# Kernel tuning notes

Hardware: AMD Instinct MI355X
Metric: run time of the kernel (lower is better)

Reference implementation:

```python
import jax, jax.numpy as jnp
import numpy as np

BLOCK_SIZE = 256
N_EMBD = 768
HEAD_SIZE = 768  # == n_embd so RoPE table (dim=n_embd) matches channel pairing


def _rope_tables(T, dim, theta0=10000.0):
    # compute_freq(dim=n_embd, seq_len=block_size, theta_0=10000):
    # theta_j = theta0^(-2j/dim), angle[t, j] = t * theta_j
    j = jnp.arange(dim // 2, dtype=jnp.float32)
    theta = jnp.float32(theta0) ** (-2.0 * j / jnp.float32(dim))
    ang = jnp.arange(T, dtype=jnp.float32)[:, None] * theta[None, :]  # [T, dim/2]
    return jnp.cos(ang), jnp.sin(ang)


def _apply_rope(t, cos, sin):
    # t: [B, T, D]; pair adjacent channels (2j, 2j+1) as complex, rotate.
    B, T, D = t.shape
    tr = t.reshape(B, T, D // 2, 2)
    re, im = tr[..., 0], tr[..., 1]
    out_re = re * cos[None] - im * sin[None]
    out_im = re * sin[None] + im * cos[None]
    return jnp.stack([out_re, out_im], axis=-1).reshape(B, T, D)


def setup_inputs() -> dict:
    key = jax.random.key(0)
    k1, k2, k3, k4 = jax.random.split(key, 4)
    B, T = 128, BLOCK_SIZE
    x = jax.random.normal(k1, (B, T, N_EMBD), dtype=jnp.float32)
    Wq = jax.random.normal(k2, (N_EMBD, HEAD_SIZE), dtype=jnp.float32) * 0.02
    Wk = jax.random.normal(k3, (N_EMBD, HEAD_SIZE), dtype=jnp.float32) * 0.02
    Wv = jax.random.normal(k4, (N_EMBD, HEAD_SIZE), dtype=jnp.float32) * 0.02
    return {"x": x, "Wq": Wq, "Wk": Wk, "Wv": Wv}


def reference(x, Wq, Wk, Wv):
    B, T, C = x.shape
    q = x @ Wq  # [B, T, D]
    k = x @ Wk
    v = x @ Wv
    cos, sin = _rope_tables(T, HEAD_SIZE)
    q = _apply_rope(q, cos, sin)
    k = _apply_rope(k, cos, sin)
    scale = jnp.float32(HEAD_SIZE) ** -0.5
    wei = jnp.einsum('bqd,bkd->bqk', q, k) * scale  # [B, T, T]
    causal = jnp.tril(jnp.ones((T, T), dtype=bool))
    wei = jnp.where(causal[None], wei, -jnp.inf)
    wei = jax.nn.softmax(wei, axis=-1)
    # dropout(p=0.2) is identity in eval/deterministic baseline
    out = jnp.einsum('bqk,bkd->bqd', wei, v)  # [B, T, D]
    return out
```

## Files before the change

### kernel.cpp

```cpp
#include <hip/hip_runtime.h>
#include <hip/hip_bf16.h>
#include <stdint.h>


typedef __attribute__((ext_vector_type(8))) short short8;
typedef __attribute__((ext_vector_type(4))) short short4v;
typedef __attribute__((ext_vector_type(4))) float f32x4;

__device__ __forceinline__ short f2bf(float f) {
    uint32_t u = __float_as_uint(f);
    u += 0x7fffu + ((u >> 16) & 1u);
    return (short)(u >> 16);
}

__global__ __launch_bounds__(256) void cvt_x(const float* __restrict__ x,
                                             short* __restrict__ xb) {
    long i = ((long)blockIdx.x * 256 + threadIdx.x) * 4;
    f32x4 v = *(const f32x4*)(x + i);
    short4v o;
    o.x = f2bf(v.x); o.y = f2bf(v.y); o.z = f2bf(v.z); o.w = f2bf(v.w);
    *(short4v*)(xb + i) = o;
}

__global__ __launch_bounds__(256) void cvt_wt(const float* __restrict__ W,
                                              short* __restrict__ Wt) {
    __shared__ float tile[32][33];
    int d0 = blockIdx.x * 32, c0 = blockIdx.y * 32;
    int tr = threadIdx.x >> 5, tc = threadIdx.x & 31;
    #pragma unroll
    for (int i = 0; i < 32; i += 8)
        tile[tr + i][tc] = W[(long)(c0 + tr + i) * 768 + d0 + tc];
    __syncthreads();
    #pragma unroll
    for (int i = 0; i < 32; i += 8)
        Wt[(long)(d0 + tr + i) * 768 + c0 + tc] = f2bf(tile[tc][tr + i]);
}

__global__ __launch_bounds__(256) void rope_tab(float2* __restrict__ rt) {
    int i = blockIdx.x * 256 + threadIdx.x;
    int t = i / 384, j = i - t * 384;
    const float CE = -0.034603417655f;
    float th = exp2f((float)j * CE);
    float s, c;
    sincosf((float)t * th, &s, &c);
    rt[i] = make_float2(c, s);
}

__global__ __launch_bounds__(512, 2)
void qkv256(const short* __restrict__ A, const short* __restrict__ B,
            short* __restrict__ Q, short* __restrict__ Kb,
            short* __restrict__ Vt, const float2* __restrict__ rt) {
    int p = blockIdx.x;
    int c = p & 7, j = p >> 3;
    int st = j / 9;
    int bx = j - st * 9;
    int by = c * 16 + st;
    const int m0 = by * 256, n0 = bx * 256;

    __shared__ short lA[2][256 * 64];
    __shared__ short lB[2][256 * 64];

    const int tid = threadIdx.x;
    const int w = tid >> 6, lane = tid & 63;
    const int wm = (w >> 2) * 128;
    const int wn = (w & 3) * 64;
    const int lr8 = lane >> 3;
    const int scol = (((lane & 7) - lr8) & 7) * 8;
    const int fr = lane & 15, kq = lane >> 4;

    f32x4 acc[8][4] = {};
    short8 af[4][2];
    short8 bq[4][2];

#define STAGE_HALF(lX, gX, r0g, h, t) do {                                     \
    int _buf = (t) & 1;                                                        \
    _Pragma("unroll")                                                          \
    for (int _i = 0; _i < 2; ++_i) {                                           \
        int _rl = (h) * 128 + (w * 2 + _i) * 8;                                \
        const short* _g = (gX) + (long)((r0g) + _rl + lr8) * 768               \
                               + (t) * 64 + scol;                              \
        __builtin_amdgcn_global_load_lds(                                      \
            (const __attribute__((address_space(1))) void*)_g,                 \
            (__attribute__((address_space(3))) void*)(&lX[_buf][_rl * 64]),    \
            16, 0, 0);                                                         \
    }                                                                          \
} while (0)

#define LOAD_A(mh, buf) do {                                                   \
    _Pragma("unroll")                                                          \
    for (int _t = 0; _t < 4; ++_t)                                             \
        _Pragma("unroll")                                                      \
        for (int _k = 0; _k < 2; ++_k)                                         \
            af[_t][_k] = *(const short8*)(&lA[buf][                            \
                (wm + (mh) * 64 + _t * 16 + fr) * 64 +                         \
                ((_k * 4 + kq + fr) & 7) * 8]);                                \
} while (0)

#define LOAD_B(nh, buf) do {                                                   \
    _Pragma("unroll")                                                          \
    for (int _t = 0; _t < 2; ++_t)                                             \
        _Pragma("unroll")                                                      \
        for (int _k = 0; _k < 2; ++_k)                                         \
            bq[(nh) * 2 + _t][_k] = *(const short8*)(&lB[buf][                 \
                (wn + (nh) * 32 + _t * 16 + fr) * 64 +                         \
                ((_k * 4 + kq + fr) & 7) * 8]);                                \
} while (0)

#define MMA_Q(mh, nh) do {                                                     \
    __builtin_amdgcn_s_setprio(1);                                             \
    _Pragma("unroll")                                                          \
    for (int _t = 0; _t < 4; ++_t)                                             \
        _Pragma("unroll")                                                      \
        for (int _n = 0; _n < 2; ++_n)                                         \
            _Pragma("unroll")                                                  \
            for (int _k = 0; _k < 2; ++_k)                                     \
                acc[(mh) * 4 + _t][(nh) * 2 + _n] =                            \
                    __builtin_amdgcn_mfma_f32_16x16x32_bf16(                   \
                        af[_t][_k], bq[(nh) * 2 + _n][_k],                     \
                        acc[(mh) * 4 + _t][(nh) * 2 + _n], 0, 0, 0);           \
    __builtin_amdgcn_s_setprio(0);                                             \
} while (0)

#define BAR() __builtin_amdgcn_s_barrier()
#define LGKM0() asm volatile("s_waitcnt lgkmcnt(0)" ::: "memory")
#define VMC4() asm volatile("s_waitcnt vmcnt(4)" ::: "memory")
#define VMC0() asm volatile("s_waitcnt vmcnt(0)" ::: "memory")

    STAGE_HALF(lB, B, n0, 0, 0);
    STAGE_HALF(lB, B, n0, 1, 0);
    STAGE_HALF(lA, A, m0, 0, 0);
    STAGE_HALF(lA, A, m0, 1, 0);
    STAGE_HALF(lB, B, n0, 0, 1);
    STAGE_HALF(lB, B, n0, 1, 1);
    VMC4();
    BAR();

    #pragma unroll 1
    for (int i = 0; i < 6; ++i) {
        const int t0 = 2 * i;
        const bool more = (i < 5);
        LOAD_A(0, 0); LOAD_B(0, 0);
        STAGE_HALF(lA, A, m0, 0, t0 + 1);
        BAR(); LGKM0(); MMA_Q(0, 0); BAR();
        LOAD_B(1, 0);
        STAGE_HALF(lA, A, m0, 1, t0 + 1);
        BAR(); LGKM0(); MMA_Q(0, 1); BAR();
        LOAD_A(1, 0);
        if (more) STAGE_HALF(lB, B, n0, 0, t0 + 2);
        BAR(); LGKM0(); MMA_Q(1, 1); BAR();
        if (more) { STAGE_HALF(lB, B, n0, 1, t0 + 2); VMC4(); }
        else      { VMC0(); }
        BAR(); LGKM0(); MMA_Q(1, 0); BAR();
        LOAD_A(0, 1); LOAD_B(0, 1);
        if (more) STAGE_HALF(lA, A, m0, 0, t0 + 2);
        BAR(); LGKM0(); MMA_Q(0, 0); BAR();
        LOAD_B(1, 1);
        if (more) STAGE_HALF(lA, A, m0, 1, t0 + 2);
        BAR(); LGKM0(); MMA_Q(0, 1); BAR();
        LOAD_A(1, 1);
        if (more) STAGE_HALF(lB, B, n0, 0, t0 + 3);
        BAR(); LGKM0(); MMA_Q(1, 1); BAR();
        if (more) { STAGE_HALF(lB, B, n0, 1, t0 + 3); VMC4(); }
        BAR(); LGKM0(); MMA_Q(1, 0); BAR();
    }

    const int type = (bx >= 6) ? 2 : (bx >= 3 ? 1 : 0);
    const int nl0 = n0 - type * 768;
    const int r0 = wm + (lane >> 4) * 4;
    const int c0 = wn + (lane & 15);
    if (type < 2) {
        short* dst = (type == 0) ? Q : Kb;
        const int par = lane & 1;
        #pragma unroll
        for (int tmi = 0; tmi < 8; ++tmi)
            #pragma unroll
            for (int tni = 0; tni < 4; ++tni) {
                int col = nl0 + c0 + tni * 16;
                const float2* rtc = rt + (col >> 1);
                #pragma unroll
                for (int r = 0; r < 4; ++r) {
                    int row = m0 + r0 + tmi * 16 + r;
                    float val = acc[tmi][tni][r];
                    float pv = __shfl_xor(val, 1);
                    float2 cs = rtc[(row & 255) * 384];
                    float re = par ? pv : val;
                    float im = par ? val : pv;
                    float o = par ? (re * cs.y + im * cs.x)
                                  : (re * cs.x - im * cs.y);
                    dst[(long)row * 768 + col] = f2bf(o);
                }
            }
    } else {
        #pragma unroll
        for (int tmi = 0; tmi < 8; ++tmi)
            #pragma unroll
            for (int tni = 0; tni < 4; ++tni) {
                int col = nl0 + c0 + tni * 16;
                #pragma unroll
                for (int r = 0; r < 4; ++r) {
                    int row = m0 + r0 + tmi * 16 + r;
                    Vt[((long)(row >> 8) * 768 + col) * 256 + (row & 255)] =
                        f2bf(acc[tmi][tni][r]);
                }
            }
    }
#undef STAGE_HALF
#undef LOAD_A
#undef LOAD_B
#undef MMA_Q
#undef BAR
#undef LGKM0
#undef VMC4
#undef VMC0
}

template <int EPI, int CAUSAL, int SWZ>
__global__ __launch_bounds__(256)
void gemm_bt(const short* __restrict__ A, const short* __restrict__ B,
             void* __restrict__ C, void* __restrict__ C2, void* __restrict__ C3,
             const float2* __restrict__ rt,
             int M, int N, int K, long sA, long sB, long sC, float scale) {
    int bx, by, bz;
    if (SWZ == 2) {
        int p = blockIdx.x + 2 * (blockIdx.y + 2 * blockIdx.z);
        int c = p & 7, j = p >> 3;
        bz = c * 16 + (j >> 2);
        by = (j >> 1) & 1; bx = j & 1;
    } else if (SWZ == 3) {
        int p = blockIdx.x + 6 * (blockIdx.y + 2 * blockIdx.z);
        int c = p & 7, j = p >> 3;
        int bt = j / 12;
        bz = c * 16 + bt;
        int t = j - bt * 12;
        by = t / 6; bx = t - (t / 6) * 6;
    } else {
        bx = blockIdx.x; by = blockIdx.y; bz = blockIdx.z;
    }
    const int m0 = by * 128;
    const int n0 = bx * 128;
    if (CAUSAL == 1 && n0 > m0) return;

    __shared__ short lA[128 * 64];
    __shared__ short lB[128 * 64];
    const short* Ab = A + (long)bz * sA;
    const short* Bb = B + (long)bz * sB;
    const int tid = threadIdx.x;
    const int w = tid >> 6, lane = tid & 63;
    const int wm = (w >> 1) * 64;
    const int wn = (w & 1) * 64;
    const int lrow8 = lane >> 3;
    const int lcol = (((lane & 7) - lrow8) & 7) * 8;
    const int fr = lane & 15;
    const int kq = lane >> 4;

    const int Kend = (CAUSAL == 2) ? (m0 + 128 < K ? m0 + 128 : K) : K;

    f32x4 acc[4][4] = {};

    for (int k0 = 0; k0 < Kend; k0 += 64) {
        #pragma unroll
        for (int i = 0; i < 4; ++i) {
            int seg = i * 4 + w;
            int row = seg * 8 + lrow8;
            const short* ga = Ab + (long)(m0 + row) * K + k0 + lcol;
            __builtin_amdgcn_global_load_lds(
                (const __attribute__((address_space(1))) void*)ga,
                (__attribute__((address_space(3))) void*)(lA + seg * 512),
                16, 0, 0);
            const short* gb = Bb + (long)(n0 + row) * K + k0 + lcol;
            __builtin_amdgcn_global_load_lds(
                (const __attribute__((address_space(1))) void*)gb,
                (__attribute__((address_space(3))) void*)(lB + seg * 512),
                16, 0, 0);
        }
        __syncthreads();

        #pragma unroll
        for (int c = 0; c < 2; ++c) {
            const int sphys = ((c * 4 + kq + fr) & 7) * 8;
            short8 afr[4], bfr[4];
            #pragma unroll
            for (int tmi = 0; tmi < 4; ++tmi)
                afr[tmi] = *(const short8*)(lA + (wm + fr + tmi * 16) * 64 + sphys);
            #pragma unroll
            for (int tni = 0; tni < 4; ++tni)
                bfr[tni] = *(const short8*)(lB + (wn + fr + tni * 16) * 64 + sphys);
            #pragma unroll
            for (int tmi = 0; tmi < 4; ++tmi)
                #pragma unroll
                for (int tni = 0; tni < 4; ++tni)
                    acc[tmi][tni] = __builtin_amdgcn_mfma_f32_16x16x32_bf16(
                        afr[tmi], bfr[tni], acc[tmi][tni], 0, 0, 0);
        }
        __syncthreads();
    }

    const int r0 = wm + (lane >> 4) * 4;
    const int c0 = wn + (lane & 15);

    if (EPI == 2) {
        #pragma unroll
        for (int tmi = 0; tmi < 4; ++tmi)
            #pragma unroll
            for (int tni = 0; tni < 4; ++tni)
                #pragma unroll
                for (int r = 0; r < 4; ++r) {
                    int row = m0 + r0 + tmi * 16 + r;
                    int col = n0 + c0 + tni * 16;
                    ((float*)C)[(long)bz * sC + (long)row * N + col] =
                        acc[tmi][tni][r] * scale;
                }
    }
}

__global__ __launch_bounds__(256) void softmax_p(const float* __restrict__ S,
                                                 short* __restrict__ P) {
    int wv = threadIdx.x >> 6, lane = threadIdx.x & 63;
    int row = blockIdx.x * 4 + wv;
    int t = row & 255;
    f32x4 v = *(const f32x4*)(S + (long)row * 256 + lane * 4);
    float vals[4];
    float m = -1e30f;
    #pragma unroll
    for (int j = 0; j < 4; ++j) {
        int n = lane * 4 + j;
        vals[j] = (n <= t) ? v[j] : -1e30f;
        m = fmaxf(m, vals[j]);
    }
    #pragma unroll
    for (int o = 32; o; o >>= 1) m = fmaxf(m, __shfl_xor(m, o));
    float e[4], sum = 0.f;
    #pragma unroll
    for (int j = 0; j < 4; ++j) { e[j] = __expf(vals[j] - m); sum += e[j]; }
    #pragma unroll
    for (int o = 32; o; o >>= 1) sum += __shfl_xor(sum, o);
    float inv = 1.0f / sum;
    short4v o4;
    o4.x = f2bf(e[0] * inv); o4.y = f2bf(e[1] * inv);
    o4.z = f2bf(e[2] * inv); o4.w = f2bf(e[3] * inv);
    *(short4v*)(P + (long)row * 256 + lane * 4) = o4;
}

extern "C" void kernel_launch(void* const* d_in, const int* in_sizes, int n_in,
                              void* d_out, int out_size, void* d_ws, size_t ws_size,
                              hipStream_t stream) {
    const float* x  = (const float*)d_in[0];
    const float* Wq = (const float*)d_in[1];
    const float* Wk = (const float*)d_in[2];
    const float* Wv = (const float*)d_in[3];

    char* ws = (char*)d_ws;
    short*  xb = (short*)(ws);
    short*  wt = (short*)(ws + 50331648);
    short*  qb = (short*)(ws + 53870592);
    short*  kb = (short*)(ws + 104202240);
    short*  vt = (short*)(ws + 154533888);
    float*  S  = (float*)(ws + 204865536);
    short*  P  = (short*)(ws + 238419968);
    float2* rt = (float2*)(ws + 255197184);

    cvt_x<<<24576, 256, 0, stream>>>(x, xb);
    dim3 gw(24, 24);
    cvt_wt<<<gw, 256, 0, stream>>>(Wq, wt);
    cvt_wt<<<gw, 256, 0, stream>>>(Wk, wt + 589824);
    cvt_wt<<<gw, 256, 0, stream>>>(Wv, wt + 1179648);
    rope_tab<<<384, 256, 0, stream>>>(rt);

    qkv256<<<1152, 512, 0, stream>>>(xb, wt, qb, kb, vt, rt);

    dim3 g2(2, 2, 128);
    gemm_bt<2, 1, 2><<<g2, 256, 0, stream>>>(qb, kb, S, nullptr, nullptr, nullptr,
                                             256, 256, 768, 196608, 196608, 65536,
                                             0.0360843918f);

    softmax_p<<<8192, 256, 0, stream>>>(S, P);

    dim3 g3(6, 2, 128);
    gemm_bt<2, 2, 3><<<g3, 256, 0, stream>>>(P, vt, (float*)d_out, nullptr,
                                             nullptr, nullptr, 256, 768, 256,
                                             65536, 196608, 196608, 1.0f);
}
```

Measured before the change: 412.5 us.

## Fuse QK^T score GEMM with causal softmax into one kernel

Replaces the separate causal QK^T GEMM (which wrote fp32 scores) and the row-softmax kernel with one kernel. Each 512-thread block computes a 128x256 score tile, masks it, and does the row max and sum reductions through LDS before writing bf16 probabilities. This removes the fp32 S round trip through global memory and one launch, but the block computes the fully masked upper tile instead of skipping it, and only 256 blocks are launched. The QKV GEMM loop also moves its vmcnt wait to after the last MFMA quarter so loads overlap more compute.

Result: no change. 412.1 us (-0.1%).

```diff
diff --git a/kernel.cpp b/kernel.cpp
--- a/kernel.cpp
+++ b/kernel.cpp
@@ -148,9 +148,10 @@
         LOAD_A(1, 0);
         if (more) STAGE_HALF(lB, B, n0, 0, t0 + 2);
         BAR(); LGKM0(); MMA_Q(1, 1); BAR();
-        if (more) { STAGE_HALF(lB, B, n0, 1, t0 + 2); VMC4(); }
-        else      { VMC0(); }
-        BAR(); LGKM0(); MMA_Q(1, 0); BAR();
+        if (more) STAGE_HALF(lB, B, n0, 1, t0 + 2);
+        BAR(); LGKM0(); MMA_Q(1, 0);
+        if (more) { VMC4(); } else { VMC0(); }
+        BAR();
         LOAD_A(0, 1); LOAD_B(0, 1);
         if (more) STAGE_HALF(lA, A, m0, 0, t0 + 2);
         BAR(); LGKM0(); MMA_Q(0, 0); BAR();
@@ -160,8 +161,10 @@
         LOAD_A(1, 1);
         if (more) STAGE_HALF(lB, B, n0, 0, t0 + 3);
         BAR(); LGKM0(); MMA_Q(1, 1); BAR();
-        if (more) { STAGE_HALF(lB, B, n0, 1, t0 + 3); VMC4(); }
-        BAR(); LGKM0(); MMA_Q(1, 0); BAR();
+        if (more) STAGE_HALF(lB, B, n0, 1, t0 + 3);
+        BAR(); LGKM0(); MMA_Q(1, 0);
+        if (more) VMC4();
+        BAR();
     }
 
     const int type = (bx >= 6) ? 2 : (bx >= 3 ? 1 : 0);
@@ -214,6 +217,153 @@
 #undef VMC0
 }
 
+__global__ __launch_bounds__(512)
+void s_softmax(const short* __restrict__ Qm, const short* __restrict__ Km,
+               short* __restrict__ P, float scale) {
+    int p = blockIdx.x;
+    int c = p & 7, j = p >> 3;
+    int bz = c * 16 + (j >> 1);
+    int mh = j & 1;
+    const short* Ab = Qm + (long)bz * 196608 + (long)mh * 98304;
+    const short* Bb = Km + (long)bz * 196608;
+
+    __shared__ short lA[128 * 64];
+    __shared__ short lB[256 * 64];
+
+    const int tid = threadIdx.x;
+    const int w = tid >> 6, lane = tid & 63;
+    const int wm = (w >> 2) * 64;
+    const int wn = (w & 3) * 64;
+    const int lr8 = lane >> 3;
+    const int scol = (((lane & 7) - lr8) & 7) * 8;
+    const int fr = lane & 15, kq = lane >> 4;
+
+    f32x4 acc[4][4] = {};
+
+    for (int k0 = 0; k0 < 768; k0 += 64) {
+        #pragma unroll
+        for (int i = 0; i < 2; ++i) {
+            int seg = i * 8 + w;
+            const short* ga = Ab + (long)(seg * 8 + lr8) * 768 + k0 + scol;
+            __builtin_amdgcn_global_load_lds(
+                (const __attribute__((address_space(1))) void*)ga,
+                (__attribute__((address_space(3))) void*)(lA + seg * 512),
+                16, 0, 0);
+        }
+        #pragma unroll
+        for (int i = 0; i < 4; ++i) {
+            int seg = i * 8 + w;
+            const short* gb = Bb + (long)(seg * 8 + lr8) * 768 + k0 + scol;
+            __builtin_amdgcn_global_load_lds(
+                (const __attribute__((address_space(1))) void*)gb,
+                (__attribute__((address_space(3))) void*)(lB + seg * 512),
+                16, 0, 0);
+        }
+        __syncthreads();
+        #pragma unroll
+        for (int cc = 0; cc < 2; ++cc) {
+            const int sphys = ((cc * 4 + kq + fr) & 7) * 8;
+            short8 afr[4], bfr[4];
+            #pragma unroll
+            for (int tmi = 0; tmi < 4; ++tmi)
+                afr[tmi] = *(const short8*)(lA + (wm + fr + tmi * 16) * 64 + sphys);
+            #pragma unroll
+            for (int tni = 0; tni < 4; ++tni)
+                bfr[tni] = *(const short8*)(lB + (wn + fr + tni * 16) * 64 + sphys);
+            #pragma unroll
+            for (int tmi = 0; tmi < 4; ++tmi)
+                #pragma unroll
+                for (int tni = 0; tni < 4; ++tni)
+                    acc[tmi][tni] = __builtin_amdgcn_mfma_f32_16x16x32_bf16(
+                        afr[tmi], bfr[tni], acc[tmi][tni], 0, 0, 0);
+        }
+        __syncthreads();
+    }
+
+    const int r0 = (lane >> 4) * 4;
+    const int cb = lane & 15;
+    const int nw = w & 3;
+    float* redm = (float*)lA;
+    float* reds = redm + 512;
+
+    float M[16];
+    #pragma unroll
+    for (int tmi = 0; tmi < 4; ++tmi)
+        #pragma unroll
+        for (int r = 0; r < 4; ++r) {
+            int rowL = wm + tmi * 16 + r0 + r;
+            int tloc = mh * 128 + rowL;
+            float m = -1e30f;
+            #pragma unroll
+            for (int tni = 0; tni < 4; ++tni) {
+                int col = wn + cb + tni * 16;
+                float v = (col <= tloc) ? acc[tmi][tni][r] * scale : -1e30f;
+                acc[tmi][tni][r] = v;
+                m = fmaxf(m, v);
+            }
+            m = fmaxf(m, __shfl_xor(m, 1));
+            m = fmaxf(m, __shfl_xor(m, 2));
+            m = fmaxf(m, __shfl_xor(m, 4));
+            m = fmaxf(m, __shfl_xor(m, 8));
+            M[tmi * 4 + r] = m;
+        }
+    if (cb == 0) {
+        #pragma unroll
+        for (int tmi = 0; tmi < 4; ++tmi)
+            #pragma unroll
+            for (int r = 0; r < 4; ++r)
+                redm[(wm + tmi * 16 + r0 + r) * 4 + nw] = M[tmi * 4 + r];
+    }
+    __syncthreads();
+    #pragma unroll
+    for (int tmi = 0; tmi < 4; ++tmi)
+        #pragma unroll
+        for (int r = 0; r < 4; ++r) {
+            f32x4 v = *(const f32x4*)(redm + (wm + tmi * 16 + r0 + r) * 4);
+            M[tmi * 4 + r] = fmaxf(fmaxf(v.x, v.y), fmaxf(v.z, v.w));
+        }
+    float Sm[16];
+    #pragma unroll
+    for (int tmi = 0; tmi < 4; ++tmi)
+        #pragma unroll
+        for (int r = 0; r < 4; ++r) {
+            float mm = M[tmi * 4 + r];
+            float s = 0.f;
+            #pragma unroll
+            for (int tni = 0; tni < 4; ++tni) {
+                float e = __expf(acc[tmi][tni][r] - mm);
+                acc[tmi][tni][r] = e;
+                s += e;
+            }
+            s += __shfl_xor(s, 1);
+            s += __shfl_xor(s, 2);
+            s += __shfl_xor(s, 4);
+            s += __shfl_xor(s, 8);
+            Sm[tmi * 4 + r] = s;
+        }
+    if (cb == 0) {
+        #pragma unroll
+        for (int tmi = 0; tmi < 4; ++tmi)
+            #pragma unroll
+            for (int r = 0; r < 4; ++r)
+                reds[(wm + tmi * 16 + r0 + r) * 4 + nw] = Sm[tmi * 4 + r];
+    }
+    __syncthreads();
+    const long rowBase = (long)bz * 256 + mh * 128;
+    #pragma unroll
+    for (int tmi = 0; tmi < 4; ++tmi)
+        #pragma unroll
+        for (int r = 0; r < 4; ++r) {
+            int rowL = wm + tmi * 16 + r0 + r;
+            f32x4 v = *(const f32x4*)(reds + rowL * 4);
+            float inv = 1.0f / (v.x + v.y + v.z + v.w);
+            short* pr = P + (rowBase + rowL) * 256;
+            #pragma unroll
+            for (int tni = 0; tni < 4; ++tni)
+                pr[wn + cb + tni * 16] = f2bf(acc[tmi][tni][r] * inv);
+        }
+}
+
 template <int EPI, int CAUSAL, int SWZ>
 __global__ __launch_bounds__(256)
 void gemm_bt(const short* __restrict__ A, const short* __restrict__ B,
@@ -221,12 +371,7 @@
              const float2* __restrict__ rt,
              int M, int N, int K, long sA, long sB, long sC, float scale) {
     int bx, by, bz;
-    if (SWZ == 2) {
-        int p = blockIdx.x + 2 * (blockIdx.y + 2 * blockIdx.z);
-        int c = p & 7, j = p >> 3;
-        bz = c * 16 + (j >> 2);
-        by = (j >> 1) & 1; bx = j & 1;
-    } else if (SWZ == 3) {
+    if (SWZ == 3) {
         int p = blockIdx.x + 6 * (blockIdx.y + 2 * blockIdx.z);
         int c = p & 7, j = p >> 3;
         int bt = j / 12;
@@ -313,34 +458,6 @@
     }
 }
 
-__global__ __launch_bounds__(256) void softmax_p(const float* __restrict__ S,
-                                                 short* __restrict__ P) {
-    int wv = threadIdx.x >> 6, lane = threadIdx.x & 63;
-    int row = blockIdx.x * 4 + wv;
-    int t = row & 255;
-    f32x4 v = *(const f32x4*)(S + (long)row * 256 + lane * 4);
-    float vals[4];
-    float m = -1e30f;
-    #pragma unroll
-    for (int j = 0; j < 4; ++j) {
-        int n = lane * 4 + j;
-        vals[j] = (n <= t) ? v[j] : -1e30f;
-        m = fmaxf(m, vals[j]);
-    }
-    #pragma unroll
-    for (int o = 32; o; o >>= 1) m = fmaxf(m, __shfl_xor(m, o));
-    float e[4], sum = 0.f;
-    #pragma unroll
-    for (int j = 0; j < 4; ++j) { e[j] = __expf(vals[j] - m); sum += e[j]; }
-    #pragma unroll
-    for (int o = 32; o; o >>= 1) sum += __shfl_xor(sum, o);
-    float inv = 1.0f / sum;
-    short4v o4;
-    o4.x = f2bf(e[0] * inv); o4.y = f2bf(e[1] * inv);
-    o4.z = f2bf(e[2] * inv); o4.w = f2bf(e[3] * inv);
-    *(short4v*)(P + (long)row * 256 + lane * 4) = o4;
-}
-
 extern "C" void kernel_launch(void* const* d_in, const int* in_sizes, int n_in,
                               void* d_out, int out_size, void* d_ws, size_t ws_size,
                               hipStream_t stream) {
@@ -355,7 +472,6 @@
     short*  qb = (short*)(ws + 53870592);
     short*  kb = (short*)(ws + 104202240);
     short*  vt = (short*)(ws + 154533888);
-    float*  S  = (float*)(ws + 204865536);
     short*  P  = (short*)(ws + 238419968);
     float2* rt = (float2*)(ws + 255197184);
 
@@ -368,12 +484,7 @@
 
     qkv256<<<1152, 512, 0, stream>>>(xb, wt, qb, kb, vt, rt);
 
-    dim3 g2(2, 2, 128);
-    gemm_bt<2, 1, 2><<<g2, 256, 0, stream>>>(qb, kb, S, nullptr, nullptr, nullptr,
-                                             256, 256, 768, 196608, 196608, 65536,
-                                             0.0360843918f);
-
-    softmax_p<<<8192, 256, 0, stream>>>(S, P);
+    s_softmax<<<256, 512, 0, stream>>>(qb, kb, P, 0.0360843918f);
 
     dim3 g3(6, 2, 128);
     gemm_bt<2, 2, 3><<<g3, 256, 0, stream>>>(P, vt, (float*)d_out, nullptr,
```
